# Performance work log

Hardware: AMD Instinct MI355X
Metric: run time of the kernel (lower is better)

The kernel has to match this reference:

```python
import jax, jax.numpy as jnp
import numpy as np

T, B, S = 64, 128, 128
H = 200   # hidden_size
E = 200   # embedding_size
A = 100   # attention projection width
V = 10003 # vocab_size


def setup_inputs() -> dict:
    key = jax.random.key(0)
    ks = jax.random.split(key, 20)
    def n(k, shape, scale):
        return (jax.random.normal(k, shape, jnp.float32) * scale).astype(jnp.float32)
    return {
        "tokens": jax.random.randint(ks[0], (T, B), 0, V),
        "hidden": n(ks[1], (1, B, H), 0.1),
        "encoder_outputs": n(ks[2], (S, B, H), 1.0),
        "emb": n(ks[3], (V, E), 0.05),
        "W1": n(ks[4], (A, H), 0.07), "b1": n(ks[5], (A,), 0.07),
        "W2": n(ks[6], (A, H), 0.07), "b2": n(ks[7], (A,), 0.07),
        "W3": n(ks[8], (A, E), 0.07), "b3": n(ks[9], (A,), 0.07),
        "attn_W": n(ks[10], (1, A), 0.1), "attn_b": n(ks[11], (1,), 0.1),
        "gru_Wih": n(ks[12], (3 * H, E + H), 0.05), "gru_Whh": n(ks[13], (3 * H, H), 0.05),
        "gru_bih": n(ks[14], (3 * H,), 0.05), "gru_bhh": n(ks[15], (3 * H,), 0.05),
        "out_W": n(ks[16], (V, H), 0.05), "out_b": n(ks[17], (V,), 0.05),
    }


def reference(tokens, hidden, encoder_outputs, emb, W1, b1, W2, b2, W3, b3,
              attn_W, attn_b, gru_Wih, gru_Whh, gru_bih, gru_bhh, out_W, out_b):
    # eval mode: dropout is identity
    enc = jnp.transpose(encoder_outputs, (1, 0, 2))   # [B, S, H]
    embedded = emb[tokens]                            # [T, B, E]
    ah3 = embedded @ W3.T + b3                        # [T, B, A] (precomputed, as in torch)
    ah2 = enc @ W2.T + b2                             # [B, S, A]
    h0 = hidden[0]                                    # [B, H]

    def step(h, xs):
        emb_t, ah3_t = xs                             # [B,E], [B,A]
        ah1 = h @ W1.T + b1                           # [B, A]
        e = jax.nn.relu(ah1[:, None, :] + ah2 + ah3_t[:, None, :])  # [B, S, A]
        logits = (e @ attn_W.T + attn_b)[..., 0]      # [B, S]
        a = jax.nn.softmax(logits, axis=1)            # [B, S]
        ctx = jnp.einsum('bs,bsh->bh', a, enc)        # [B, H]
        x = jnp.concatenate([emb_t, ctx], axis=1)     # [B, E+H]
        gi = x @ gru_Wih.T + gru_bih                  # [B, 3H]
        gh = h @ gru_Whh.T + gru_bhh                  # [B, 3H]
        ir, iz, in_ = jnp.split(gi, 3, axis=1)
        hr, hz, hn = jnp.split(gh, 3, axis=1)
        r = jax.nn.sigmoid(ir + hr)
        z = jax.nn.sigmoid(iz + hz)
        nn_ = jnp.tanh(in_ + r * hn)
        h_new = (1.0 - z) * nn_ + z * h               # [B, H]
        logp = jax.nn.log_softmax(h_new @ out_W.T + out_b, axis=1)  # [B, V]
        return h_new, (logp, a)

    h_last, (outputs, attns) = jax.lax.scan(step, h0, (embedded, ah3))
    # outputs [T,B,V]; hidden [1,B,H]; attentions [T,B,1,S] (torch's view(B,1,S) per step)
    return outputs, h_last[None], attns[:, :, None, :]
```

## Files before the change

### kernel.cpp

```cpp
#include <hip/hip_runtime.h>
#include <hip/hip_bf16.h>
#include <cmath>

constexpr int T_ = 64, B_ = 128, S_ = 128, H_ = 200, E_ = 200, A_ = 100, V_ = 10003;
constexpr int KP = 224;
constexpr int VP = 10240;
constexpr int MROWS = T_ * B_;
constexpr int NCB = VP / 256;
constexpr int G3 = 3 * H_;
constexpr int EH = E_ + H_;
constexpr int ELD = 136;
constexpr int AH2P = 104;

typedef __attribute__((ext_vector_type(8))) short bf16x8;
typedef __attribute__((ext_vector_type(4))) float f32x4;
typedef __attribute__((ext_vector_type(2))) _Float16 h2;
typedef __attribute__((ext_vector_type(8))) _Float16 h8;

#if __has_builtin(__builtin_amdgcn_fdot2)
__device__ __forceinline__ float fdot2f(h2 a, h2 b, float c) {
  return __builtin_amdgcn_fdot2(a, b, c, false);
}
#else
__device__ __forceinline__ float fdot2f(h2 a, h2 b, float c) {
  return c + (float)a[0] * (float)b[0] + (float)a[1] * (float)b[1];
}
#endif

__device__ __forceinline__ float dot200h(const h8* __restrict__ w, int n, int stride,
                                         const h8* __restrict__ x) {
  float a0 = 0.f, a1 = 0.f, a2 = 0.f, a3 = 0.f;
#pragma unroll
  for (int k8 = 0; k8 < 25; ++k8) {
    h8 wv = w[k8 * stride + n];
    h8 xv = x[k8];
    h2 wp[4], xp[4];
    __builtin_memcpy(wp, &wv, 16);
    __builtin_memcpy(xp, &xv, 16);
    a0 = fdot2f(wp[0], xp[0], a0);
    a1 = fdot2f(wp[1], xp[1], a1);
    a2 = fdot2f(wp[2], xp[2], a2);
    a3 = fdot2f(wp[3], xp[3], a3);
  }
  return (a0 + a1) + (a2 + a3);
}

__device__ __forceinline__ float dot200p5(const h8* __restrict__ w, int stride,
                                          const h8* __restrict__ x) {
  const h8* p = w;
  h8 w0 = p[0]; p += stride;
  h8 w1 = p[0]; p += stride;
  h8 w2 = p[0]; p += stride;
  h8 w3 = p[0]; p += stride;
  h8 w4 = p[0]; p += stride;
  float a0 = 0.f, a1 = 0.f, a2 = 0.f, a3 = 0.f;
#define DOT_CONSUME(WREG, K)                    \
  {                                             \
    h8 xv = x[K];                               \
    h2 wp[4], xp[4];                            \
    __builtin_memcpy(wp, &WREG, 16);            \
    __builtin_memcpy(xp, &xv, 16);              \
    a0 = fdot2f(wp[0], xp[0], a0);              \
    a1 = fdot2f(wp[1], xp[1], a1);              \
    a2 = fdot2f(wp[2], xp[2], a2);              \
    a3 = fdot2f(wp[3], xp[3], a3);              \
  }
#define DOT_RELOAD(WREG) { WREG = p[0]; p += stride; }
  DOT_CONSUME(w0, 0)  DOT_RELOAD(w0)
  DOT_CONSUME(w1, 1)  DOT_RELOAD(w1)
  DOT_CONSUME(w2, 2)  DOT_RELOAD(w2)
  DOT_CONSUME(w3, 3)  DOT_RELOAD(w3)
  DOT_CONSUME(w4, 4)  DOT_RELOAD(w4)
  DOT_CONSUME(w0, 5)  DOT_RELOAD(w0)
  DOT_CONSUME(w1, 6)  DOT_RELOAD(w1)
  DOT_CONSUME(w2, 7)  DOT_RELOAD(w2)
  DOT_CONSUME(w3, 8)  DOT_RELOAD(w3)
  DOT_CONSUME(w4, 9)  DOT_RELOAD(w4)
  DOT_CONSUME(w0, 10) DOT_RELOAD(w0)
  DOT_CONSUME(w1, 11) DOT_RELOAD(w1)
  DOT_CONSUME(w2, 12) DOT_RELOAD(w2)
  DOT_CONSUME(w3, 13) DOT_RELOAD(w3)
  DOT_CONSUME(w4, 14) DOT_RELOAD(w4)
  DOT_CONSUME(w0, 15) DOT_RELOAD(w0)
  DOT_CONSUME(w1, 16) DOT_RELOAD(w1)
  DOT_CONSUME(w2, 17) DOT_RELOAD(w2)
  DOT_CONSUME(w3, 18) DOT_RELOAD(w3)
  DOT_CONSUME(w4, 19) DOT_RELOAD(w4)
  DOT_CONSUME(w0, 20)
  DOT_CONSUME(w1, 21)
  DOT_CONSUME(w2, 22)
  DOT_CONSUME(w3, 23)
  DOT_CONSUME(w4, 24)
#undef DOT_CONSUME
#undef DOT_RELOAD
  return (a0 + a1) + (a2 + a3);
}


__global__ __launch_bounds__(256) void k_pack(const float* __restrict__ outW,
                                              const float* __restrict__ W1,
                                              const float* __restrict__ Wih,
                                              const float* __restrict__ Whh,
                                              __hip_bfloat16* __restrict__ wpk,
                                              __hip_bfloat16* __restrict__ hall,
                                              _Float16* __restrict__ W1h,
                                              _Float16* __restrict__ Wihh,
                                              _Float16* __restrict__ Whhh) {
  const int stride = gridDim.x * blockDim.x;
  const int tid0 = blockIdx.x * blockDim.x + threadIdx.x;
  const int total = (KP / 8) * VP * 8;
  for (int idx = tid0; idx < total; idx += stride) {
    int kk = idx & 7;
    int v = (idx >> 3) % VP;
    int kb = idx / (8 * VP);
    int k = kb * 8 + kk;
    float val = (k < H_ && v < V_) ? outW[(size_t)v * H_ + k] : 0.f;
    wpk[idx] = __float2bfloat16(val);
  }
  const __hip_bfloat16 z = __float2bfloat16(0.f);
  for (int idx = tid0; idx < MROWS * (KP - H_); idx += stride) {
    int row = idx / (KP - H_), col = H_ + idx % (KP - H_);
    hall[(size_t)row * KP + col] = z;
  }
  for (int idx = tid0; idx < 25 * A_ * 8; idx += stride) {
    int kk = idx & 7, a = (idx >> 3) % A_, k8 = idx / (8 * A_);
    W1h[idx] = (_Float16)W1[(size_t)a * H_ + k8 * 8 + kk];
  }
  for (int idx = tid0; idx < 50 * G3 * 8; idx += stride) {
    int kk = idx & 7, n = (idx >> 3) % G3, k8 = idx / (8 * G3);
    Wihh[idx] = (_Float16)Wih[(size_t)n * EH + k8 * 8 + kk];
  }
  for (int idx = tid0; idx < 25 * G3 * 8; idx += stride) {
    int kk = idx & 7, n = (idx >> 3) % G3, k8 = idx / (8 * G3);
    Whhh[idx] = (_Float16)Whh[(size_t)n * H_ + k8 * 8 + kk];
  }
}

__global__ __launch_bounds__(256) void k_ah2(const float* __restrict__ encoder,
                                             const float* __restrict__ W2,
                                             const float* __restrict__ b2,
                                             _Float16* __restrict__ ah2h) {
  __shared__ float encL[16][200];
  const int s = blockIdx.x, b0 = blockIdx.y * 16, tid = threadIdx.x;
  for (int i = tid; i < 16 * 200; i += 256) {
    int bl = i / 200, k = i % 200;
    encL[bl][k] = encoder[((size_t)s * B_ + b0 + bl) * H_ + k];
  }
  __syncthreads();
  for (int o = tid; o < 16 * A_; o += 256) {
    int bl = o / A_, a = o % A_;
    const float* w = W2 + (size_t)a * H_;
    float acc = b2[a];
    for (int k = 0; k < H_; ++k) acc += encL[bl][k] * w[k];
    ah2h[((size_t)(b0 + bl) * S_ + s) * AH2P + a] = (_Float16)acc;
  }
  for (int o = tid; o < 16 * (AH2P - A_); o += 256) {
    int bl = o / (AH2P - A_), a = A_ + o % (AH2P - A_);
    ah2h[((size_t)(b0 + bl) * S_ + s) * AH2P + a] = (_Float16)0.f;
  }
}

__global__ __launch_bounds__(256) void k_ah3(const int* __restrict__ tokens,
                                             const float* __restrict__ emb,
                                             const float* __restrict__ W3,
                                             const float* __restrict__ b3,
                                             float* __restrict__ ah3) {
  __shared__ float embL[16][200];
  __shared__ int tokL[16];
  const int t = blockIdx.x, b0 = blockIdx.y * 16, tid = threadIdx.x;
  if (tid < 16) tokL[tid] = tokens[t * B_ + b0 + tid];
  __syncthreads();
  for (int i = tid; i < 16 * 200; i += 256) {
    int bl = i / 200, k = i % 200;
    embL[bl][k] = emb[(size_t)tokL[bl] * E_ + k];
  }
  __syncthreads();
  for (int o = tid; o < 16 * A_; o += 256) {
    int bl = o / A_, a = o % A_;
    const float* w = W3 + (size_t)a * E_;
    float acc = b3[a];
    for (int k = 0; k < E_; ++k) acc += embL[bl][k] * w[k];
    ah3[((size_t)t * B_ + b0 + bl) * A_ + a] = acc;
  }
}

__global__ __launch_bounds__(512) void k_gix(const int* __restrict__ tokens,
                                             const float* __restrict__ emb,
                                             const _Float16* __restrict__ Wihh,
                                             const float* __restrict__ bih,
                                             float* __restrict__ giX) {
  __shared__ __align__(16) _Float16 xeL[16][208];
  __shared__ int tokL[16];
  const int t = blockIdx.x, b0 = blockIdx.y * 16, tid = threadIdx.x;
  if (tid < 16) tokL[tid] = tokens[t * B_ + b0 + tid];
  __syncthreads();
  for (int i = tid; i < 16 * 200; i += 512) {
    int bl = i / 200, k = i % 200;
    xeL[bl][k] = (_Float16)emb[(size_t)tokL[bl] * E_ + k];
  }
  __syncthreads();
  const h8* W8 = (const h8*)Wihh;
  for (int u = tid; u < 16 * G3; u += 512) {
    int bl = u / G3, n = u - bl * G3;
    float acc = dot200h(W8, n, G3, (const h8*)&xeL[bl][0]) + bih[n];
    giX[((size_t)t * B_ + b0 + bl) * G3 + n] = acc;
  }
}

__global__ __launch_bounds__(512) void k_recur(const float* __restrict__ hidden0,
                                               const _Float16* __restrict__ ah2h,
                                               const float* __restrict__ ah3,
                                               const float* __restrict__ encoder,
                                               const _Float16* __restrict__ W1h,
                                               const float* __restrict__ b1,
                                               const float* __restrict__ attn_W,
                                               const float* __restrict__ attn_b,
                                               const _Float16* __restrict__ Wihh,
                                               const _Float16* __restrict__ Whhh,
                                               const float* __restrict__ bhh,
                                               const float* __restrict__ giX,
                                               __hip_bfloat16* __restrict__ hall,
                                               float* __restrict__ out_hidden,
                                               float* __restrict__ out_attn) {
  __shared__ __align__(16) _Float16 encLh[H_ * ELD];
  __shared__ __align__(16) h2 h16[100];
  __shared__ __align__(16) h2 xch[100];
  __shared__ __align__(16) h2 aLh[64];
  __shared__ float s1[AH2P];
  __shared__ float aW[AH2P];
  __shared__ float red[8];
  __shared__ float giL[G3];
  __shared__ float part[1200];

  const int b = blockIdx.x, tid = threadIdx.x;
  const int lane = tid & 63;

  for (int i = tid; i < S_ * H_; i += 512) {
    int s = i / H_, h = i - s * H_;
    encLh[h * ELD + s] = (_Float16)encoder[((size_t)s * B_ + b) * H_ + h];
  }
  float hreg = 0.f, bhr = 0.f, bhz = 0.f, bhn = 0.f;
  if (tid < H_) {
    hreg = hidden0[b * H_ + tid];
    bhr = bhh[tid]; bhz = bhh[200 + tid]; bhn = bhh[400 + tid];
  }
  if (tid < 100) {
    h2 v;
    v[0] = (_Float16)hidden0[b * H_ + 2 * tid];
    v[1] = (_Float16)hidden0[b * H_ + 2 * tid + 1];
    h16[tid] = v;
  }
  for (int i = tid; i < AH2P; i += 512) {
    aW[i] = (i < A_) ? attn_W[i] : 0.f;
    s1[i] = 0.f;
  }
  h8 ah2row[13];
  if (tid < S_) {
    const h8* src = (const h8*)(ah2h + ((size_t)b * S_ + tid) * AH2P);
#pragma unroll
    for (int r = 0; r < 13; ++r) ah2row[r] = src[r];
  }
  const float ab = attn_b[0];
  __syncthreads();

  const h8* W1h8 = (const h8*)W1h;
  const h8* Wihc8 = (const h8*)Wihh + (size_t)25 * G3;
  const h8* Whhh8 = (const h8*)Whhh;

  for (int t = 0; t < T_; ++t) {
    const h8* xs = (const h8*)h16;
    for (int u = tid; u < 700; u += 512) {
      if (u < 100) {
        const float ah3A = ah3[((size_t)t * B_ + b) * A_ + u];
        const float b1A = b1[u];
        s1[u] = dot200p5(W1h8 + u, A_, xs) + b1A + ah3A;
      } else {
        const int g = u - 100;
        part[g] = dot200p5(Whhh8 + g, G3, xs);
      }
    }
    __syncthreads();

    float evw = 0.f;
    const int w01 = tid >> 6;
    if (tid < S_) {
      float acc = ab;
#pragma unroll
      for (int r = 0; r < 13; ++r) {
        h8 w = ah2row[r];
#pragma unroll
        for (int j = 0; j < 8; ++j) {
          const int a = r * 8 + j;
          acc += fmaxf(s1[a] + (float)w[j], 0.f) * aW[a];
        }
      }
      float m = acc;
#pragma unroll
      for (int off = 32; off > 0; off >>= 1) m = fmaxf(m, __shfl_xor(m, off, 64));
      evw = expf(acc - m);
      float sm = evw;
#pragma unroll
      for (int off = 32; off > 0; off >>= 1) sm += __shfl_xor(sm, off, 64);
      if (lane == 0) { red[w01] = m; red[4 + w01] = sm; }
    }
    __syncthreads();
    if (tid < S_) {
      const float m0 = red[0], m1 = red[1];
      const float M = fmaxf(m0, m1);
      const float SS = red[4] * expf(m0 - M) + red[5] * expf(m1 - M);
      const float av = evw * expf((w01 ? m1 : m0) - M) / SS;
      out_attn[((size_t)t * B_ + b) * S_ + tid] = av;
      const float avn = __shfl_xor(av, 1, 64);
      if ((tid & 1) == 0) {
        h2 v; v[0] = (_Float16)av; v[1] = (_Float16)avn;
        aLh[tid >> 1] = v;
      }
    }
    __syncthreads();

    if (tid < H_) {
      const h8* er = (const h8*)(encLh + tid * ELD);
      float c0 = 0.f, c1 = 0.f, c2 = 0.f, c3 = 0.f;
#pragma unroll
      for (int k8 = 0; k8 < 16; ++k8) {
        h8 evv = er[k8];
        h2 ep[4];
        __builtin_memcpy(ep, &evv, 16);
        c0 = fdot2f(ep[0], aLh[4 * k8 + 0], c0);
        c1 = fdot2f(ep[1], aLh[4 * k8 + 1], c1);
        c2 = fdot2f(ep[2], aLh[4 * k8 + 2], c2);
        c3 = fdot2f(ep[3], aLh[4 * k8 + 3], c3);
      }
      const float c = (c0 + c1) + (c2 + c3);
      const float cn = __shfl_xor(c, 1, 64);
      if ((tid & 1) == 0) {
        h2 v; v[0] = (_Float16)c; v[1] = (_Float16)cn;
        xch[tid >> 1] = v;
      }
    } else {
      const int j = tid - 200;
      if (j < 300) {
        float2 g2 = ((const float2*)(giX + ((size_t)t * B_ + b) * G3))[j];
        giL[2 * j] = g2.x;
        giL[2 * j + 1] = g2.y;
      }
    }
    __syncthreads();

    {
      const h8* xc8 = (const h8*)xch;
      for (int u = tid; u < 600; u += 512) {
        part[600 + u] = dot200p5(Wihc8 + u, G3, xc8);
      }
    }
    __syncthreads();

    if (tid < H_) {
      const int n = tid;
      const float gir = giL[n] + part[600 + n];
      const float giz = giL[200 + n] + part[800 + n];
      const float gin = giL[400 + n] + part[1000 + n];
      const float ghr = part[n] + bhr;
      const float ghz = part[200 + n] + bhz;
      const float ghn = part[400 + n] + bhn;
      const float r = 1.f / (1.f + expf(-(gir + ghr)));
      const float z = 1.f / (1.f + expf(-(giz + ghz)));
      const float nn = tanhf(gin + r * ghn);
      const float hv = (1.f - z) * nn + z * hreg;
      hreg = hv;
      hall[((size_t)t * B_ + b) * KP + n] = __float2bfloat16(hv);
      const float hn2 = __shfl_xor(hv, 1, 64);
      if ((n & 1) == 0) {
        h2 v; v[0] = (_Float16)hv; v[1] = (_Float16)hn2;
        h16[n >> 1] = v;
      }
      if (t == T_ - 1) out_hidden[b * H_ + n] = hv;
    }
    __syncthreads();
  }
}

__global__ __launch_bounds__(256) void k_big0(const short* __restrict__ hb,
                                              const short* __restrict__ wpk,
                                              const float* __restrict__ outb,
                                              float* __restrict__ pmax,
                                              float* __restrict__ psum) {
  const int tid = threadIdx.x;
  const int w = tid >> 6, l = tid & 63;
  const int lm = l & 15, lg = l >> 4;
  const int r0 = blockIdx.y * 64;
  const int v0 = blockIdx.x * 256 + w * 64;

  f32x4 acc[4][4] = {};
#pragma unroll
  for (int kt = 0; kt < KP / 32; ++kt) {
    const int k0 = kt * 32;
    bf16x8 af[4], bfr[4];
#pragma unroll
    for (int wm = 0; wm < 4; ++wm)
      af[wm] = *(const bf16x8*)(hb + (size_t)(r0 + wm * 16 + lm) * KP + k0 + lg * 8);
#pragma unroll
    for (int n = 0; n < 4; ++n)
      bfr[n] = *(const bf16x8*)(wpk + ((size_t)((k0 >> 3) + lg) * VP + v0 + n * 16 + lm) * 8);
#pragma unroll
    for (int wm = 0; wm < 4; ++wm)
#pragma unroll
      for (int n = 0; n < 4; ++n)
        acc[wm][n] = __builtin_amdgcn_mfma_f32_16x16x32_bf16(af[wm], bfr[n], acc[wm][n], 0, 0, 0);
  }

  int vv[4]; float bias[4]; bool val[4];
#pragma unroll
  for (int n = 0; n < 4; ++n) {
    vv[n] = v0 + n * 16 + lm;
    val[n] = vv[n] < V_;
    bias[n] = val[n] ? outb[vv[n]] : 0.f;
  }

  __shared__ float smax[4][64], ssum[4][64];
#pragma unroll
  for (int wm = 0; wm < 4; ++wm) {
#pragma unroll
    for (int j = 0; j < 4; ++j) {
      float mv = -INFINITY;
#pragma unroll
      for (int n = 0; n < 4; ++n)
        if (val[n]) mv = fmaxf(mv, acc[wm][n][j] + bias[n]);
      for (int off = 8; off > 0; off >>= 1) mv = fmaxf(mv, __shfl_xor(mv, off, 64));
      float sv = 0.f;
#pragma unroll
      for (int n = 0; n < 4; ++n)
        if (val[n]) sv += expf(acc[wm][n][j] + bias[n] - mv);
      for (int off = 8; off > 0; off >>= 1) sv += __shfl_xor(sv, off, 64);
      if (lm == 0) {
        smax[w][wm * 16 + lg * 4 + j] = mv;
        ssum[w][wm * 16 + lg * 4 + j] = sv;
      }
    }
  }
  __syncthreads();
  if (tid < 64) {
    float mv = -INFINITY;
    for (int ww = 0; ww < 4; ++ww) mv = fmaxf(mv, smax[ww][tid]);
    float sv = 0.f;
    for (int ww = 0; ww < 4; ++ww) {
      float sw = ssum[ww][tid];
      if (sw > 0.f) sv += expf(smax[ww][tid] - mv) * sw;
    }
    pmax[(size_t)blockIdx.x * MROWS + r0 + tid] = mv;
    psum[(size_t)blockIdx.x * MROWS + r0 + tid] = sv;
  }
}

__global__ __launch_bounds__(256) void k_lse(const float* __restrict__ pmax,
                                             const float* __restrict__ psum,
                                             float* __restrict__ lse) {
  const int r = blockIdx.x * 256 + threadIdx.x;
  float mv = -INFINITY;
  for (int c = 0; c < NCB; ++c) mv = fmaxf(mv, pmax[(size_t)c * MROWS + r]);
  float sv = 0.f;
  for (int c = 0; c < NCB; ++c) {
    float sw = psum[(size_t)c * MROWS + r];
    if (sw > 0.f) sv += expf(pmax[(size_t)c * MROWS + r] - mv) * sw;
  }
  lse[r] = mv + logf(sv);
}

__global__ __launch_bounds__(256) void k_big1(const short* __restrict__ hb,
                                              const short* __restrict__ wpk,
                                              const float* __restrict__ outb,
                                              const float* __restrict__ lse,
                                              float* __restrict__ out_logp) {
  const int tid = threadIdx.x;
  const int w = tid >> 6, l = tid & 63;
  const int lm = l & 15, lg = l >> 4;
  const int r0 = blockIdx.y * 64;
  const int v0 = blockIdx.x * 256 + w * 64;

  __shared__ float lseL[64];
  if (tid < 64) lseL[tid] = lse[r0 + tid];

  f32x4 acc[4][4] = {};
#pragma unroll
  for (int kt = 0; kt < KP / 32; ++kt) {
    const int k0 = kt * 32;
    bf16x8 af[4], bfr[4];
#pragma unroll
    for (int wm = 0; wm < 4; ++wm)
      af[wm] = *(const bf16x8*)(hb + (size_t)(r0 + wm * 16 + lm) * KP + k0 + lg * 8);
#pragma unroll
    for (int n = 0; n < 4; ++n)
      bfr[n] = *(const bf16x8*)(wpk + ((size_t)((k0 >> 3) + lg) * VP + v0 + n * 16 + lm) * 8);
#pragma unroll
    for (int wm = 0; wm < 4; ++wm)
#pragma unroll
      for (int n = 0; n < 4; ++n)
        acc[wm][n] = __builtin_amdgcn_mfma_f32_16x16x32_bf16(af[wm], bfr[n], acc[wm][n], 0, 0, 0);
  }

  int vv[4]; float bias[4]; bool val[4];
#pragma unroll
  for (int n = 0; n < 4; ++n) {
    vv[n] = v0 + n * 16 + lm;
    val[n] = vv[n] < V_;
    bias[n] = val[n] ? outb[vv[n]] : 0.f;
  }
  __syncthreads();
#pragma unroll
  for (int wm = 0; wm < 4; ++wm) {
#pragma unroll
    for (int j = 0; j < 4; ++j) {
      const int row = r0 + wm * 16 + lg * 4 + j;
      const float ls = lseL[wm * 16 + lg * 4 + j];
#pragma unroll
      for (int n = 0; n < 4; ++n)
        if (val[n]) out_logp[(size_t)row * V_ + vv[n]] = acc[wm][n][j] + bias[n] - ls;
    }
  }
}


extern "C" void kernel_launch(void* const* d_in, const int* in_sizes, int n_in,
                              void* d_out, int out_size, void* d_ws, size_t ws_size,
                              hipStream_t stream) {
  (void)in_sizes; (void)n_in; (void)out_size; (void)ws_size;
  const int* tokens = (const int*)d_in[0];
  const float* hidden0 = (const float*)d_in[1];
  const float* encoder = (const float*)d_in[2];
  const float* emb = (const float*)d_in[3];
  const float* W1 = (const float*)d_in[4];
  const float* b1 = (const float*)d_in[5];
  const float* W2 = (const float*)d_in[6];
  const float* b2 = (const float*)d_in[7];
  const float* W3 = (const float*)d_in[8];
  const float* b3 = (const float*)d_in[9];
  const float* attn_W = (const float*)d_in[10];
  const float* attn_b = (const float*)d_in[11];
  const float* Wih = (const float*)d_in[12];
  const float* Whh = (const float*)d_in[13];
  const float* bih = (const float*)d_in[14];
  const float* bhh = (const float*)d_in[15];
  const float* outW = (const float*)d_in[16];
  const float* outb = (const float*)d_in[17];

  float* out_logp = (float*)d_out;
  float* out_hidden = out_logp + (size_t)T_ * B_ * V_;
  float* out_attn = out_hidden + (size_t)B_ * H_;

  float* ws = (float*)d_ws;
  float* ah3w = ws;
  float* pmaxw = ah3w + (size_t)T_ * B_ * A_;
  float* psumw = pmaxw + (size_t)NCB * MROWS;
  float* lsew = psumw + (size_t)NCB * MROWS;
  float* giXw = lsew + MROWS;
  __hip_bfloat16* hallw = (__hip_bfloat16*)(giXw + (size_t)MROWS * G3);
  __hip_bfloat16* wpkw = hallw + (size_t)MROWS * KP;
  _Float16* ah2hw = (_Float16*)(wpkw + (size_t)(KP / 8) * VP * 8);
  _Float16* W1hw = ah2hw + (size_t)B_ * S_ * AH2P;
  _Float16* Wihhw = W1hw + (size_t)25 * A_ * 8;
  _Float16* Whhhw = Wihhw + (size_t)50 * G3 * 8;

  k_pack<<<512, 256, 0, stream>>>(outW, W1, Wih, Whh, wpkw, hallw, W1hw, Wihhw, Whhhw);
  k_ah2<<<dim3(S_, B_ / 16), 256, 0, stream>>>(encoder, W2, b2, ah2hw);
  k_ah3<<<dim3(T_, B_ / 16), 256, 0, stream>>>(tokens, emb, W3, b3, ah3w);
  k_gix<<<dim3(T_, B_ / 16), 512, 0, stream>>>(tokens, emb, Wihhw, bih, giXw);

  k_recur<<<B_, 512, 0, stream>>>(hidden0, ah2hw, ah3w, encoder, W1hw, b1, attn_W,
                                  attn_b, Wihhw, Whhhw, bhh, giXw,
                                  hallw, out_hidden, out_attn);

  k_big0<<<dim3(NCB, MROWS / 64), 256, 0, stream>>>((const short*)hallw, (const short*)wpkw,
                                                    outb, pmaxw, psumw);
  k_lse<<<MROWS / 256, 256, 0, stream>>>(pmaxw, psumw, lsew);
  k_big1<<<dim3(NCB, MROWS / 64), 256, 0, stream>>>((const short*)hallw, (const short*)wpkw,
                                                    outb, lsew, out_logp);
}
```

Before: 1.114 ms.

## Fuse embedding projections for GRU input and attention into one MFMA GEMM

Replaces the two scalar pre-pass kernels (k_ah3 computing emb@W3 and k_gix computing emb@Wih[:, :E]) with a single bf16 MFMA GEMM over a packed, concatenated weight [Wih_emb | W3] padded to 768 columns. The pack kernel builds the combined bf16 weight layout. This removes one launch and moves the FLOP-heavy projections onto matrix cores. In exchange, the embedding inputs are rounded to bf16 instead of fp16/fp32, which lowers precision of giX and ah3.

```diff
diff --git a/kernel.cpp b/kernel.cpp
--- a/kernel.cpp
+++ b/kernel.cpp
@@ -11,6 +11,7 @@
 constexpr int EH = E_ + H_;
 constexpr int ELD = 136;
 constexpr int AH2P = 104;
+constexpr int NP = 768;
 
 typedef __attribute__((ext_vector_type(8))) short bf16x8;
 typedef __attribute__((ext_vector_type(4))) float f32x4;
@@ -26,24 +27,6 @@
   return c + (float)a[0] * (float)b[0] + (float)a[1] * (float)b[1];
 }
 #endif
-
-__device__ __forceinline__ float dot200h(const h8* __restrict__ w, int n, int stride,
-                                         const h8* __restrict__ x) {
-  float a0 = 0.f, a1 = 0.f, a2 = 0.f, a3 = 0.f;
-#pragma unroll
-  for (int k8 = 0; k8 < 25; ++k8) {
-    h8 wv = w[k8 * stride + n];
-    h8 xv = x[k8];
-    h2 wp[4], xp[4];
-    __builtin_memcpy(wp, &wv, 16);
-    __builtin_memcpy(xp, &xv, 16);
-    a0 = fdot2f(wp[0], xp[0], a0);
-    a1 = fdot2f(wp[1], xp[1], a1);
-    a2 = fdot2f(wp[2], xp[2], a2);
-    a3 = fdot2f(wp[3], xp[3], a3);
-  }
-  return (a0 + a1) + (a2 + a3);
-}
 
 __device__ __forceinline__ float dot200p5(const h8* __restrict__ w, int stride,
                                           const h8* __restrict__ x) {
@@ -101,11 +84,13 @@
                                               const float* __restrict__ W1,
                                               const float* __restrict__ Wih,
                                               const float* __restrict__ Whh,
+                                              const float* __restrict__ W3,
                                               __hip_bfloat16* __restrict__ wpk,
                                               __hip_bfloat16* __restrict__ hall,
                                               _Float16* __restrict__ W1h,
                                               _Float16* __restrict__ Wihh,
-                                              _Float16* __restrict__ Whhh) {
+                                              _Float16* __restrict__ Whhh,
+                                              __hip_bfloat16* __restrict__ wep) {
   const int stride = gridDim.x * blockDim.x;
   const int tid0 = blockIdx.x * blockDim.x + threadIdx.x;
   const int total = (KP / 8) * VP * 8;
@@ -134,6 +119,16 @@
     int kk = idx & 7, n = (idx >> 3) % G3, k8 = idx / (8 * G3);
     Whhh[idx] = (_Float16)Whh[(size_t)n * H_ + k8 * 8 + kk];
   }
+  for (int idx = tid0; idx < (KP / 8) * NP * 8; idx += stride) {
+    int kk = idx & 7, c = (idx >> 3) % NP, k8 = idx / (8 * NP);
+    int k = k8 * 8 + kk;
+    float v = 0.f;
+    if (k < E_) {
+      if (c < G3) v = Wih[(size_t)c * EH + k];
+      else if (c < G3 + A_) v = W3[(size_t)(c - G3) * E_ + k];
+    }
+    wep[idx] = __float2bfloat16(v);
+  }
 }
 
 __global__ __launch_bounds__(256) void k_ah2(const float* __restrict__ encoder,
@@ -160,50 +155,64 @@
   }
 }
 
-__global__ __launch_bounds__(256) void k_ah3(const int* __restrict__ tokens,
-                                             const float* __restrict__ emb,
-                                             const float* __restrict__ W3,
-                                             const float* __restrict__ b3,
-                                             float* __restrict__ ah3) {
-  __shared__ float embL[16][200];
-  __shared__ int tokL[16];
-  const int t = blockIdx.x, b0 = blockIdx.y * 16, tid = threadIdx.x;
-  if (tid < 16) tokL[tid] = tokens[t * B_ + b0 + tid];
+__global__ __launch_bounds__(256) void k_gemb(const int* __restrict__ tokens,
+                                              const float* __restrict__ emb,
+                                              const short* __restrict__ wep,
+                                              const float* __restrict__ bih,
+                                              const float* __restrict__ b3,
+                                              float* __restrict__ giX,
+                                              float* __restrict__ ah3) {
+  constexpr int ALD = 232;
+  __shared__ __align__(16) __hip_bfloat16 aL[64 * ALD];
+  __shared__ int tokL[64];
+  const int tid = threadIdx.x;
+  const int w = tid >> 6, l = tid & 63, lm = l & 15, lg = l >> 4;
+  const int r0 = blockIdx.y * 64;
+  const int v0 = blockIdx.x * 256 + w * 64;
+
+  if (tid < 64) tokL[tid] = tokens[r0 + tid];
   __syncthreads();
-  for (int i = tid; i < 16 * 200; i += 256) {
-    int bl = i / 200, k = i % 200;
-    embL[bl][k] = emb[(size_t)tokL[bl] * E_ + k];
+  for (int i = tid; i < 64 * KP; i += 256) {
+    int row = i / KP, k = i - row * KP;
+    float v = (k < E_) ? emb[(size_t)tokL[row] * E_ + k] : 0.f;
+    aL[row * ALD + k] = __float2bfloat16(v);
   }
   __syncthreads();
-  for (int o = tid; o < 16 * A_; o += 256) {
-    int bl = o / A_, a = o % A_;
-    const float* w = W3 + (size_t)a * E_;
-    float acc = b3[a];
-    for (int k = 0; k < E_; ++k) acc += embL[bl][k] * w[k];
-    ah3[((size_t)t * B_ + b0 + bl) * A_ + a] = acc;
-  }
-}
-
-__global__ __launch_bounds__(512) void k_gix(const int* __restrict__ tokens,
-                                             const float* __restrict__ emb,
-                                             const _Float16* __restrict__ Wihh,
-                                             const float* __restrict__ bih,
-                                             float* __restrict__ giX) {
-  __shared__ __align__(16) _Float16 xeL[16][208];
-  __shared__ int tokL[16];
-  const int t = blockIdx.x, b0 = blockIdx.y * 16, tid = threadIdx.x;
-  if (tid < 16) tokL[tid] = tokens[t * B_ + b0 + tid];
-  __syncthreads();
-  for (int i = tid; i < 16 * 200; i += 512) {
-    int bl = i / 200, k = i % 200;
-    xeL[bl][k] = (_Float16)emb[(size_t)tokL[bl] * E_ + k];
-  }
-  __syncthreads();
-  const h8* W8 = (const h8*)Wihh;
-  for (int u = tid; u < 16 * G3; u += 512) {
-    int bl = u / G3, n = u - bl * G3;
-    float acc = dot200h(W8, n, G3, (const h8*)&xeL[bl][0]) + bih[n];
-    giX[((size_t)t * B_ + b0 + bl) * G3 + n] = acc;
+
+  f32x4 acc[4][4] = {};
+#pragma unroll
+  for (int kt = 0; kt < KP / 32; ++kt) {
+    const int k0 = kt * 32;
+    bf16x8 af[4], bfr[4];
+#pragma unroll
+    for (int wm = 0; wm < 4; ++wm)
+      af[wm] = *(const bf16x8*)(aL + (wm * 16 + lm) * ALD + k0 + lg * 8);
+#pragma unroll
+    for (int n = 0; n < 4; ++n)
+      bfr[n] = *(const bf16x8*)(wep + ((size_t)((k0 >> 3) + lg) * NP + v0 + n * 16 + lm) * 8);
+#pragma unroll
+    for (int wm = 0; wm < 4; ++wm)
+#pragma unroll
+      for (int n = 0; n < 4; ++n)
+        acc[wm][n] = __builtin_amdgcn_mfma_f32_16x16x32_bf16(af[wm], bfr[n], acc[wm][n], 0, 0, 0);
+  }
+
+#pragma unroll
+  for (int n = 0; n < 4; ++n) {
+    const int vv = v0 + n * 16 + lm;
+    const bool isGi = vv < G3;
+    const bool isA3 = !isGi && vv < G3 + A_;
+    const float bias = isGi ? bih[vv] : (isA3 ? b3[vv - G3] : 0.f);
+#pragma unroll
+    for (int wm = 0; wm < 4; ++wm) {
+#pragma unroll
+      for (int j = 0; j < 4; ++j) {
+        const int row = r0 + wm * 16 + lg * 4 + j;
+        const float val = acc[wm][n][j] + bias;
+        if (isGi) giX[(size_t)row * G3 + vv] = val;
+        else if (isA3) ah3[(size_t)row * A_ + (vv - G3)] = val;
+      }
+    }
   }
 }
 
@@ -559,11 +568,13 @@
   _Float16* W1hw = ah2hw + (size_t)B_ * S_ * AH2P;
   _Float16* Wihhw = W1hw + (size_t)25 * A_ * 8;
   _Float16* Whhhw = Wihhw + (size_t)50 * G3 * 8;
-
-  k_pack<<<512, 256, 0, stream>>>(outW, W1, Wih, Whh, wpkw, hallw, W1hw, Wihhw, Whhhw);
+  __hip_bfloat16* wepw = (__hip_bfloat16*)(Whhhw + (size_t)25 * G3 * 8);
+
+  k_pack<<<512, 256, 0, stream>>>(outW, W1, Wih, Whh, W3, wpkw, hallw,
+                                  W1hw, Wihhw, Whhhw, wepw);
   k_ah2<<<dim3(S_, B_ / 16), 256, 0, stream>>>(encoder, W2, b2, ah2hw);
-  k_ah3<<<dim3(T_, B_ / 16), 256, 0, stream>>>(tokens, emb, W3, b3, ah3w);
-  k_gix<<<dim3(T_, B_ / 16), 512, 0, stream>>>(tokens, emb, Wihhw, bih, giXw);
+  k_gemb<<<dim3(NP / 256, MROWS / 64), 256, 0, stream>>>(tokens, emb, (const short*)wepw,
+                                                         bih, b3, giXw, ah3w);
 
   k_recur<<<B_, 512, 0, stream>>>(hidden0, ah2hw, ah3w, encoder, W1hw, b1, attn_W,
                                   attn_b, Wihhw, Whhhw, bhh, giXw,
```

Measured after the change: 1.033 ms. -7.3%, faster.
